# Kernel optimization log

Measured on AMD Instinct MI355X. Metric: run time of the kernel, lower is better.

Reference implementation:

```python
import jax, jax.numpy as jnp
import numpy as np

GAMMA = 0.5
LENS = 0.5
WINDOW = 10  # window_size from init

@jax.custom_vjp
def act_fun(x):
    # Heaviside forward, Gaussian surrogate backward (matches torch ActFun)
    return (x > 0).astype(x.dtype)

def _act_fwd(x):
    return act_fun(x), x

def _act_bwd(x, g):
    temp = jnp.exp(-x * x / (2 * LENS * LENS)) / (np.sqrt(2 * np.pi) * LENS)
    return (GAMMA * g * temp,)

act_fun.defvjp(_act_fwd, _act_bwd)

def mem_update(inputs, mem, thr):
    # decay_neu == 1
    mem = mem + inputs
    spike = act_fun(mem - thr)
    mem = mem * (1 - spike)
    neg = (mem < -thr).astype(mem.dtype)
    mem = mem * (1 - neg) - thr * neg
    return mem, spike

def setup_inputs() -> dict:
    key = jax.random.key(0)
    ks = jax.random.split(key, 6)
    B, T, D, H, O = 128, 100, 2048, 1024, 20
    return {
        "input": jax.random.normal(ks[0], (B, T, D), jnp.float32),
        "labels": jax.random.randint(ks[1], (B,), 0, O),
        "hidden_mem": jnp.zeros((B, H), jnp.float32),
        "hidden_spike": jnp.zeros((B, H), jnp.float32),
        "output_mem": jnp.zeros((B, O), jnp.float32),
        "output_spike": jnp.zeros((B, O), jnp.float32),
        "Wi2h": jax.random.normal(ks[2], (H, D), jnp.float32) / np.sqrt(D).astype(np.float32),
        "bi2h": jnp.zeros((H,), jnp.float32),
        "Wh2h": jax.random.normal(ks[3], (H, H), jnp.float32) / np.sqrt(H).astype(np.float32),
        "bh2h": jnp.zeros((H,), jnp.float32),
        "Wh2o": jax.random.normal(ks[4], (O, H), jnp.float32) / np.sqrt(H).astype(np.float32),
        "bh2o": jnp.zeros((O,), jnp.float32),
        "thr_h": jnp.ones((H,), jnp.float32),
        "thr_o": jnp.ones((O,), jnp.float32),
    }

def reference(input, labels, hidden_mem, hidden_spike, output_mem, output_spike,
              Wi2h, bi2h, Wh2h, bh2h, Wh2o, bh2o, thr_h, thr_o):
    B = input.shape[0]

    def step(carry, x_t):
        hm, hs, om, osp, osum = carry
        h_in = x_t @ Wi2h.T + bi2h + hs @ Wh2h.T + bh2h
        hm, hs = mem_update(h_in, hm, thr_h)
        om, osp = mem_update(hs @ Wh2o.T + bh2o, om, thr_o)
        osum = osum + osp
        nbr = (jnp.sum(osp) + jnp.sum(hs)) / B
        return (hm, hs, om, osp, osum), (hs, nbr)

    osum0 = jnp.zeros_like(output_spike)
    carry0 = (hidden_mem, hidden_spike, output_mem, output_spike, osum0)
    (hm, hs, om, osp, osum), (hs_t, nbr_events) = jax.lax.scan(
        step, carry0, jnp.swapaxes(input, 0, 1))  # scan over T

    hidden_spike_t = jnp.transpose(hs_t, (1, 2, 0))  # [B, H, T]
    # moving average over time windows (unfold + mean), stride 1
    c = jnp.cumsum(jnp.pad(hidden_spike_t, ((0, 0), (0, 0), (1, 0))), axis=2)
    hidden_spike_filt = (c[:, :, WINDOW:] - c[:, :, :-WINDOW]) / WINDOW  # [B,H,T-W+1]

    logp = jax.nn.log_softmax(osum, axis=1)
    predictions = jnp.argmax(logp, axis=1)[None, :]  # [1, B]
    loss = -jnp.mean(logp[jnp.arange(B), labels])  # NLLLoss on log_softmax
    return predictions, loss, nbr_events, hidden_spike_filt
```

## Files before the change

### kernel.cpp

```cpp
#include <hip/hip_runtime.h>
#include <hip/hip_bf16.h>
#include <cstdint>
#include <cstddef>

#define B_ 128
#define T_ 100
#define D_ 2048
#define H_ 1024
#define O_ 20
#define H2 512

__device__ inline void f4acc(float4& a, const float4 v) {
    a.x += v.x; a.y += v.y; a.z += v.z; a.w += v.w;
}

__global__ __launch_bounds__(256) void prep_kernel(const float* __restrict__ Wh2o,
                                                   float* __restrict__ W2oT,
                                                   float* __restrict__ nbr,
                                                   int* __restrict__ g_flag)
{
    int i = blockIdx.x * 256 + threadIdx.x;
    if (i < H_ * O_) {
        int hh = i / O_;
        int oo = i - hh * O_;
        W2oT[i] = Wh2o[oo * H_ + hh];
    }
    if (i < T_) nbr[i] = 0.0f;
    if (i < B_ * 2) g_flag[i] = 0;
}

__global__ __launch_bounds__(256) void transpose_kernel(const float* __restrict__ A,
                                                        float* __restrict__ AT)
{
    __shared__ float tile[32][33];
    int bx = blockIdx.x * 32, by = blockIdx.y * 32;
    int tx = threadIdx.x, ty = threadIdx.y;
#pragma unroll
    for (int i = 0; i < 32; i += 8)
        tile[ty + i][tx] = A[(size_t)(by + ty + i) * H_ + bx + tx];
    __syncthreads();
#pragma unroll
    for (int i = 0; i < 32; i += 8)
        AT[(size_t)(bx + ty + i) * H_ + by + tx] = tile[tx][ty + i];
}

__global__ __launch_bounds__(256) void gemm_xi_kernel(
    const float* __restrict__ X,
    const float* __restrict__ W,
    const float* __restrict__ bi2h,
    const float* __restrict__ bh2h,
    float* __restrict__ Xi)
{
    constexpr int BM = 128, BN = 128, BK = 16;
    __shared__ float As[BK][BM + 4];
    __shared__ float Bs[BK][BN + 4];
    const int tid = threadIdx.x;
    const int m0 = blockIdx.x * BM;
    const int n0 = blockIdx.y * BN;
    const int wave = tid >> 6;
    const int lane = tid & 63;
    const int tm = ((wave >> 1) << 3) | (lane >> 3);
    const int tn = ((wave & 1) << 3) | (lane & 7);
    const int ldr = tid >> 2;
    const int ldc = (tid & 3) << 2;

    float acc[8][8];
#pragma unroll
    for (int i = 0; i < 8; ++i)
#pragma unroll
        for (int j = 0; j < 8; ++j) acc[i][j] = 0.0f;

    for (int k0 = 0; k0 < D_; k0 += BK) {
#pragma unroll
        for (int p = 0; p < 2; ++p) {
            int r = ldr + p * 64;
            float4 v = *(const float4*)(X + (size_t)(m0 + r) * D_ + k0 + ldc);
            As[ldc + 0][r] = v.x; As[ldc + 1][r] = v.y;
            As[ldc + 2][r] = v.z; As[ldc + 3][r] = v.w;
        }
#pragma unroll
        for (int p = 0; p < 2; ++p) {
            int r = ldr + p * 64;
            float4 v = *(const float4*)(W + (size_t)(n0 + r) * D_ + k0 + ldc);
            Bs[ldc + 0][r] = v.x; Bs[ldc + 1][r] = v.y;
            Bs[ldc + 2][r] = v.z; Bs[ldc + 3][r] = v.w;
        }
        __syncthreads();
#pragma unroll
        for (int k = 0; k < BK; ++k) {
            float4 A0 = *(const float4*)&As[k][tm * 8];
            float4 A1 = *(const float4*)&As[k][tm * 8 + 4];
            float4 B0 = *(const float4*)&Bs[k][tn * 8];
            float4 B1 = *(const float4*)&Bs[k][tn * 8 + 4];
            float a[8] = {A0.x, A0.y, A0.z, A0.w, A1.x, A1.y, A1.z, A1.w};
            float bb[8] = {B0.x, B0.y, B0.z, B0.w, B1.x, B1.y, B1.z, B1.w};
#pragma unroll
            for (int i = 0; i < 8; ++i)
#pragma unroll
                for (int j = 0; j < 8; ++j) acc[i][j] += a[i] * bb[j];
        }
        __syncthreads();
    }

    float bsum[8];
#pragma unroll
    for (int j = 0; j < 8; ++j) {
        int n = n0 + tn * 8 + j;
        bsum[j] = bi2h[n] + bh2h[n];
    }
#pragma unroll
    for (int i = 0; i < 8; ++i) {
        size_t row = (size_t)(m0 + tm * 8 + i);
        float4 o0 = {acc[i][0] + bsum[0], acc[i][1] + bsum[1],
                     acc[i][2] + bsum[2], acc[i][3] + bsum[3]};
        float4 o1 = {acc[i][4] + bsum[4], acc[i][5] + bsum[5],
                     acc[i][6] + bsum[6], acc[i][7] + bsum[7]};
        *(float4*)(Xi + row * H_ + n0 + tn * 8)     = o0;
        *(float4*)(Xi + row * H_ + n0 + tn * 8 + 4) = o1;
    }
}

__global__ __launch_bounds__(512) void phase2_kernel(
    const float* __restrict__ Xi,
    const float* __restrict__ WT,
    const float* __restrict__ W2oT,
    const float* __restrict__ bh2o,
    const float* __restrict__ thr_h_g,
    const float* __restrict__ thr_o_g,
    const float* __restrict__ hm0,
    const float* __restrict__ hs0,
    const float* __restrict__ om0,
    unsigned long long* __restrict__ g_mask,
    int* __restrict__ g_flag,
    ulonglong2* __restrict__ spk,
    float* __restrict__ osum_out,
    float* __restrict__ nbr_acc)
{
    const int pair = blockIdx.x >> 1;
    const int half = blockIdx.x & 1;
    const int b = pair;
    const int tid = threadIdx.x;
    const int lane = tid & 63;
    const int wv = tid >> 6;
    const int h0 = half * H2;
    const int ph0 = h0 ^ H2;
    const int h = h0 + tid;

    __shared__ int   s_list[1024];
    __shared__ float4 s_red[4][128];
    __shared__ unsigned long long s_mask[16];
    __shared__ float s_opart[8][O_];
    __shared__ float s_om[O_], s_osum[O_], s_tho[O_], s_bo[O_];

    float hm = hm0[(size_t)b * H_ + h];
    const float thr = thr_h_g[h];

    if (half == 0 && tid < O_) {
        s_om[tid]   = om0[b * O_ + tid];
        s_osum[tid] = 0.0f;
        s_tho[tid]  = thr_o_g[tid];
        s_bo[tid]   = bh2o[tid];
    }

    {
        bool own = hs0[(size_t)b * H_ + h] > 0.5f;
        bool par = hs0[(size_t)b * H_ + ph0 + tid] > 0.5f;
        unsigned long long mo = __ballot(own), mp = __ballot(par);
        if (lane == 0) { s_mask[half * 8 + wv] = mo; s_mask[(half ^ 1) * 8 + wv] = mp; }
    }
    __syncthreads();

    int cnt_own;
    {
        const int ow = half * 8;
        int pc[8];
#pragma unroll
        for (int k = 0; k < 8; ++k) pc[k] = __popcll(s_mask[ow + k]);
        int basew = 0, tot = 0;
#pragma unroll
        for (int k = 0; k < 8; ++k) { if (k < wv) basew += pc[k]; tot += pc[k]; }
        cnt_own = tot;
        unsigned long long mw = s_mask[ow + wv];
        if ((mw >> lane) & 1ull)
            s_list[basew + __popcll(mw & ((1ull << lane) - 1ull))] = h;
    }
    __syncthreads();

    const float4* __restrict__ wt4b = (const float4*)WT + (h0 >> 2);
    const int g = tid >> 7;
    const int cid = tid & 127;
    const int fl_partner = pair * 2 + (half ^ 1);
    const int fl_self    = pair * 2 + half;
    unsigned long long bits0 = 0, bits1 = 0;

    for (int t = 0; t <= T_; ++t) {
        const bool full = (t < T_);
        float xi = 0.0f;
        if (full) xi = Xi[((size_t)b * T_ + t) * H_ + h];

        float4 c0 = {0,0,0,0}, c1 = {0,0,0,0}, c2 = {0,0,0,0}, c3 = {0,0,0,0};
        float4 c4 = {0,0,0,0}, c5 = {0,0,0,0}, c6 = {0,0,0,0}, c7 = {0,0,0,0};

        if (full) {
            const int c = cnt_own;
            int l = g;
            for (; l + 28 < c; l += 32) {
                int j0 = s_list[l],      j1 = s_list[l + 4];
                int j2 = s_list[l + 8],  j3 = s_list[l + 12];
                int j4 = s_list[l + 16], j5 = s_list[l + 20];
                int j6 = s_list[l + 24], j7 = s_list[l + 28];
                f4acc(c0, wt4b[(size_t)j0 * 256 + cid]);
                f4acc(c1, wt4b[(size_t)j1 * 256 + cid]);
                f4acc(c2, wt4b[(size_t)j2 * 256 + cid]);
                f4acc(c3, wt4b[(size_t)j3 * 256 + cid]);
                f4acc(c4, wt4b[(size_t)j4 * 256 + cid]);
                f4acc(c5, wt4b[(size_t)j5 * 256 + cid]);
                f4acc(c6, wt4b[(size_t)j6 * 256 + cid]);
                f4acc(c7, wt4b[(size_t)j7 * 256 + cid]);
            }
            for (; l < c; l += 4) f4acc(c0, wt4b[(size_t)s_list[l] * 256 + cid]);
        }

        if (t > 0 && tid == 0) {
            while (__hip_atomic_load(&g_flag[fl_partner], __ATOMIC_ACQUIRE,
                                     __HIP_MEMORY_SCOPE_AGENT) < t)
                __builtin_amdgcn_s_sleep(1);
        }
        __syncthreads();
        if (t > 0 && tid < 8) {
            const unsigned long long* pm =
                g_mask + (((size_t)(pair * 2 + ((t - 1) & 1)) * 2 + (half ^ 1)) * 8);
            s_mask[(half ^ 1) * 8 + tid] =
                __hip_atomic_load(&pm[tid], __ATOMIC_RELAXED, __HIP_MEMORY_SCOPE_AGENT);
        }
        __syncthreads();

        int cnt_p;
        {
            const int pw = (half ^ 1) * 8;
            int pc[8];
#pragma unroll
            for (int k = 0; k < 8; ++k) pc[k] = __popcll(s_mask[pw + k]);
            int basew = 0, tot = 0;
#pragma unroll
            for (int k = 0; k < 8; ++k) { if (k < wv) basew += pc[k]; tot += pc[k]; }
            cnt_p = tot;
            unsigned long long mw = s_mask[pw + wv];
            if ((mw >> lane) & 1ull)
                s_list[512 + basew + __popcll(mw & ((1ull << lane) - 1ull))] =
                    ph0 + wv * 64 + lane;
        }
        __syncthreads();

        if (full) {
            const int c = cnt_p;
            int l = g;
            for (; l + 28 < c; l += 32) {
                int j0 = s_list[512 + l],      j1 = s_list[512 + l + 4];
                int j2 = s_list[512 + l + 8],  j3 = s_list[512 + l + 12];
                int j4 = s_list[512 + l + 16], j5 = s_list[512 + l + 20];
                int j6 = s_list[512 + l + 24], j7 = s_list[512 + l + 28];
                f4acc(c0, wt4b[(size_t)j0 * 256 + cid]);
                f4acc(c1, wt4b[(size_t)j1 * 256 + cid]);
                f4acc(c2, wt4b[(size_t)j2 * 256 + cid]);
                f4acc(c3, wt4b[(size_t)j3 * 256 + cid]);
                f4acc(c4, wt4b[(size_t)j4 * 256 + cid]);
                f4acc(c5, wt4b[(size_t)j5 * 256 + cid]);
                f4acc(c6, wt4b[(size_t)j6 * 256 + cid]);
                f4acc(c7, wt4b[(size_t)j7 * 256 + cid]);
            }
            for (; l < c; l += 4) f4acc(c0, wt4b[(size_t)s_list[512 + l] * 256 + cid]);
        }

        if (half == 0 && t > 0 && lane < O_) {
            float op = 0.0f;
            for (int q = wv; q < cnt_own; q += 8) op += W2oT[s_list[q] * O_ + lane];
            for (int q = wv; q < cnt_p; q += 8)  op += W2oT[s_list[512 + q] * O_ + lane];
            s_opart[wv][lane] = op;
        }

        {
            f4acc(c0, c1); f4acc(c2, c3); f4acc(c4, c5); f4acc(c6, c7);
            f4acc(c0, c2); f4acc(c4, c6); f4acc(c0, c4);
            s_red[g][cid] = c0;
        }
        const int hidprev = cnt_own + cnt_p;
        __syncthreads();

        if (full) {
            const float* rf = (const float*)s_red;
            float val = rf[tid] + rf[512 + tid] + rf[1024 + tid] + rf[1536 + tid];
            hm += xi + val;
            bool sp = (hm - thr) > 0.0f;
            if (sp) hm = 0.0f;
            if (hm < -thr) hm = -thr;
            if (sp) { if (t < 64) bits0 |= 1ull << t; else bits1 |= 1ull << (t - 64); }
            unsigned long long m = __ballot(sp);
            if (lane == 0) {
                s_mask[half * 8 + wv] = m;
                unsigned long long* gm =
                    g_mask + (((size_t)(pair * 2 + (t & 1)) * 2 + half) * 8);
                __hip_atomic_store(&gm[wv], m, __ATOMIC_RELAXED,
                                   __HIP_MEMORY_SCOPE_AGENT);
            }
        }

        if (half == 0 && t > 0) {
            float osp_l = 0.0f;
            if (tid < O_) {
                float oin = s_bo[tid];
#pragma unroll
                for (int w = 0; w < 8; ++w) oin += s_opart[w][tid];
                float om = s_om[tid] + oin;
                float osp = ((om - s_tho[tid]) > 0.0f) ? 1.0f : 0.0f;
                if (osp > 0.5f) om = 0.0f;
                if (om < -s_tho[tid]) om = -s_tho[tid];
                s_om[tid] = om;
                s_osum[tid] += osp;
                osp_l = osp;
            }
            if (wv == 0) {
                float cc = osp_l;
                cc += __shfl_xor(cc, 1);  cc += __shfl_xor(cc, 2);
                cc += __shfl_xor(cc, 4);  cc += __shfl_xor(cc, 8);
                cc += __shfl_xor(cc, 16); cc += __shfl_xor(cc, 32);
                if (lane == 0)
                    atomicAdd(&nbr_acc[t - 1], cc + (float)hidprev);
            }
        }
        __syncthreads();
        if (full && tid == 0)
            __hip_atomic_store(&g_flag[fl_self], t + 1, __ATOMIC_RELEASE,
                               __HIP_MEMORY_SCOPE_AGENT);
        if (full) {
            const int ow = half * 8;
            int pc[8];
#pragma unroll
            for (int k = 0; k < 8; ++k) pc[k] = __popcll(s_mask[ow + k]);
            int basew = 0, tot = 0;
#pragma unroll
            for (int k = 0; k < 8; ++k) { if (k < wv) basew += pc[k]; tot += pc[k]; }
            cnt_own = tot;
            unsigned long long mw = s_mask[ow + wv];
            if ((mw >> lane) & 1ull)
                s_list[basew + __popcll(mw & ((1ull << lane) - 1ull))] = h;
        }
        __syncthreads();
    }

    ulonglong2 vv; vv.x = bits0; vv.y = bits1;
    spk[(size_t)b * H_ + h] = vv;
    if (half == 0 && tid < O_) osum_out[b * O_ + tid] = s_osum[tid];
}

__global__ __launch_bounds__(256) void filt_kernel(const ulonglong2* __restrict__ spk,
                                                   float* __restrict__ outf)
{
    int i = blockIdx.x * 256 + threadIdx.x;
    ulonglong2 v = spk[i];
    float* o = outf + (size_t)i * 91;
    int s = __popcll(v.x & 0x3FFull);
    o[0] = (float)s * 0.1f;
#pragma unroll 1
    for (int tau = 1; tau <= 90; ++tau) {
        int ta = tau + 9, tsb = tau - 1;
        int add = (ta < 64) ? (int)((v.x >> ta) & 1ull) : (int)((v.y >> (ta - 64)) & 1ull);
        int sub = (tsb < 64) ? (int)((v.x >> tsb) & 1ull) : (int)((v.y >> (tsb - 64)) & 1ull);
        s += add - sub;
        o[tau] = (float)s * 0.1f;
    }
}

__global__ __launch_bounds__(256) void final_kernel(const float* __restrict__ osum,
                                                    const int* __restrict__ labels,
                                                    float* __restrict__ dout)
{
    __shared__ float s_loss[B_];
    int tid = threadIdx.x;
    if (tid < B_) {
        int b = tid;
        float v[O_];
#pragma unroll
        for (int o = 0; o < O_; ++o) v[o] = osum[b * O_ + o];
        float mv = v[0];
        int am = 0;
#pragma unroll
        for (int o = 1; o < O_; ++o)
            if (v[o] > mv) { mv = v[o]; am = o; }
        float se = 0.0f;
#pragma unroll
        for (int o = 0; o < O_; ++o) se += expf(v[o] - mv);
        float lse = mv + logf(se);
        dout[b] = (float)am;
        s_loss[b] = v[labels[b]] - lse;
    }
    if (tid >= 128 && tid < 128 + T_) {
        dout[129 + (tid - 128)] *= (1.0f / (float)B_);
    }
    __syncthreads();
    if (tid == 0) {
        float s = 0.0f;
        for (int b = 0; b < B_; ++b) s += s_loss[b];
        dout[128] = -s / (float)B_;
    }
}

extern "C" void kernel_launch(void* const* d_in, const int* in_sizes, int n_in,
                              void* d_out, int out_size, void* d_ws, size_t ws_size,
                              hipStream_t stream)
{
    const float* input  = (const float*)d_in[0];
    const int*   labels = (const int*)d_in[1];
    const float* hm0    = (const float*)d_in[2];
    const float* hs0    = (const float*)d_in[3];
    const float* om0    = (const float*)d_in[4];
    const float* Wi2h   = (const float*)d_in[6];
    const float* bi2h   = (const float*)d_in[7];
    const float* Wh2h   = (const float*)d_in[8];
    const float* bh2h   = (const float*)d_in[9];
    const float* Wh2o   = (const float*)d_in[10];
    const float* bh2o   = (const float*)d_in[11];
    const float* thr_h  = (const float*)d_in[12];
    const float* thr_o  = (const float*)d_in[13];

    float* out  = (float*)d_out;
    float* nbr  = out + 129;
    float* filt = out + 229;

    char* ws = (char*)d_ws;
    float*      Xi     = (float*)(ws);
    float*      WT     = (float*)(ws + 52428800);
    float*      W2oT   = (float*)(ws + 56623104);
    ulonglong2* spk    = (ulonglong2*)(ws + 56705024);
    float*      osum   = (float*)(ws + 58802176);
    unsigned long long* g_mask = (unsigned long long*)(ws + 58812416);
    int*        g_flag  = (int*)(ws + 58845184);

    prep_kernel<<<80, 256, 0, stream>>>(Wh2o, W2oT, nbr, g_flag);
    transpose_kernel<<<dim3(32, 32), dim3(32, 8), 0, stream>>>(Wh2h, WT);
    gemm_xi_kernel<<<dim3(100, 8), 256, 0, stream>>>(input, Wi2h, bi2h, bh2h, Xi);
    phase2_kernel<<<256, 512, 0, stream>>>(Xi, WT, W2oT, bh2o, thr_h, thr_o,
                                           hm0, hs0, om0, g_mask, g_flag,
                                           spk, osum, nbr);
    filt_kernel<<<512, 256, 0, stream>>>(spk, filt);
    final_kernel<<<1, 256, 0, stream>>>(osum, labels, out);
}
```

Before: 2.027 ms.

## Fuse input GEMM into recurrent kernel with per-timestep readiness flags

Merges the input-projection GEMM and the recurrent scan into one persistent launch. The first 256 blocks run the recurrence and the other 800 each compute one timestep tile of Xi. Each GEMM block bumps a per-timestep counter, and the recurrent blocks spin on the counter for t+1 before moving on. This lets the recurrence start before the whole GEMM finishes, overlapping the two phases. The risks are forward-progress deadlock if recurrent blocks hold resources while GEMM blocks cannot schedule, plus a smaller and less efficient GEMM tile (128x128 with 512 threads per block) and contention on the compute units.

```diff
diff --git a/kernel.cpp b/kernel.cpp
--- a/kernel.cpp
+++ b/kernel.cpp
@@ -10,6 +10,12 @@
 #define O_ 20
 #define H2 512
 
+#define P2NB 256
+#define GEMM_NB 800
+#define XI_READY 8
+
+typedef float vfloat4 __attribute__((ext_vector_type(4)));
+
 __device__ inline void f4acc(float4& a, const float4 v) {
     a.x += v.x; a.y += v.y; a.z += v.z; a.w += v.w;
 }
@@ -17,7 +23,8 @@
 __global__ __launch_bounds__(256) void prep_kernel(const float* __restrict__ Wh2o,
                                                    float* __restrict__ W2oT,
                                                    float* __restrict__ nbr,
-                                                   int* __restrict__ g_flag)
+                                                   int* __restrict__ g_flag,
+                                                   int* __restrict__ xi_done)
 {
     int i = blockIdx.x * 256 + threadIdx.x;
     if (i < H_ * O_) {
@@ -25,7 +32,7 @@
         int oo = i - hh * O_;
         W2oT[i] = Wh2o[oo * H_ + hh];
     }
-    if (i < T_) nbr[i] = 0.0f;
+    if (i < T_) { nbr[i] = 0.0f; xi_done[i] = 0; }
     if (i < B_ * 2) g_flag[i] = 0;
 }
 
@@ -44,84 +51,79 @@
         AT[(size_t)(bx + ty + i) * H_ + by + tx] = tile[tx][ty + i];
 }
 
-__global__ __launch_bounds__(256) void gemm_xi_kernel(
+__device__ __forceinline__ void gemm_role(int g,
+    const float* __restrict__ X, const float* __restrict__ W,
+    const float* __restrict__ bi2h, const float* __restrict__ bh2h,
+    float* __restrict__ Xi, int* __restrict__ xi_done)
+{
+    __shared__ float As[16][132];
+    __shared__ float Bs[16][132];
+    const int t   = g >> 3;
+    const int n0  = (g & 7) << 7;
+    const int tid = threadIdx.x;
+    const int tm8 = (tid >> 5) << 3;
+    const int tn4 = (tid & 31) << 2;
+    const int ldr = tid >> 2;
+    const int ldc = (tid & 3) << 2;
+
+    const float* Xp = X + (size_t)ldr * (T_ * D_) + (size_t)t * D_ + ldc;
+    const float* Wp = W + (size_t)(n0 + ldr) * D_ + ldc;
+
+    float acc[8][4];
+#pragma unroll
+    for (int i = 0; i < 8; ++i)
+#pragma unroll
+        for (int j = 0; j < 4; ++j) acc[i][j] = 0.0f;
+
+    for (int k0 = 0; k0 < D_; k0 += 16) {
+        vfloat4 va = __builtin_nontemporal_load((const vfloat4*)(Xp + k0));
+        float4 vb = *(const float4*)(Wp + k0);
+        __syncthreads();
+        As[ldc + 0][ldr] = va.x; As[ldc + 1][ldr] = va.y;
+        As[ldc + 2][ldr] = va.z; As[ldc + 3][ldr] = va.w;
+        Bs[ldc + 0][ldr] = vb.x; Bs[ldc + 1][ldr] = vb.y;
+        Bs[ldc + 2][ldr] = vb.z; Bs[ldc + 3][ldr] = vb.w;
+        __syncthreads();
+#pragma unroll
+        for (int k = 0; k < 16; ++k) {
+            float4 A0 = *(const float4*)&As[k][tm8];
+            float4 A1 = *(const float4*)&As[k][tm8 + 4];
+            float4 B0 = *(const float4*)&Bs[k][tn4];
+            float a[8] = {A0.x, A0.y, A0.z, A0.w, A1.x, A1.y, A1.z, A1.w};
+            float b4[4] = {B0.x, B0.y, B0.z, B0.w};
+#pragma unroll
+            for (int i = 0; i < 8; ++i)
+#pragma unroll
+                for (int j = 0; j < 4; ++j) acc[i][j] += a[i] * b4[j];
+        }
+    }
+
+    float bs[4];
+#pragma unroll
+    for (int j = 0; j < 4; ++j) {
+        int n = n0 + tn4 + j;
+        bs[j] = bi2h[n] + bh2h[n];
+    }
+#pragma unroll
+    for (int i = 0; i < 8; ++i) {
+        size_t row = (size_t)(tm8 + i) * T_ + t;
+        vfloat4 o = {acc[i][0] + bs[0], acc[i][1] + bs[1],
+                     acc[i][2] + bs[2], acc[i][3] + bs[3]};
+        __builtin_nontemporal_store(o, (vfloat4*)(Xi + row * H_ + n0 + tn4));
+    }
+    __syncthreads();
+    if (tid == 0)
+        __hip_atomic_fetch_add(&xi_done[t], 1, __ATOMIC_RELEASE,
+                               __HIP_MEMORY_SCOPE_AGENT);
+}
+
+__global__ __launch_bounds__(512, 4) void mega_kernel(
     const float* __restrict__ X,
-    const float* __restrict__ W,
+    const float* __restrict__ Wi2h,
     const float* __restrict__ bi2h,
     const float* __restrict__ bh2h,
-    float* __restrict__ Xi)
-{
-    constexpr int BM = 128, BN = 128, BK = 16;
-    __shared__ float As[BK][BM + 4];
-    __shared__ float Bs[BK][BN + 4];
-    const int tid = threadIdx.x;
-    const int m0 = blockIdx.x * BM;
-    const int n0 = blockIdx.y * BN;
-    const int wave = tid >> 6;
-    const int lane = tid & 63;
-    const int tm = ((wave >> 1) << 3) | (lane >> 3);
-    const int tn = ((wave & 1) << 3) | (lane & 7);
-    const int ldr = tid >> 2;
-    const int ldc = (tid & 3) << 2;
-
-    float acc[8][8];
-#pragma unroll
-    for (int i = 0; i < 8; ++i)
-#pragma unroll
-        for (int j = 0; j < 8; ++j) acc[i][j] = 0.0f;
-
-    for (int k0 = 0; k0 < D_; k0 += BK) {
-#pragma unroll
-        for (int p = 0; p < 2; ++p) {
-            int r = ldr + p * 64;
-            float4 v = *(const float4*)(X + (size_t)(m0 + r) * D_ + k0 + ldc);
-            As[ldc + 0][r] = v.x; As[ldc + 1][r] = v.y;
-            As[ldc + 2][r] = v.z; As[ldc + 3][r] = v.w;
-        }
-#pragma unroll
-        for (int p = 0; p < 2; ++p) {
-            int r = ldr + p * 64;
-            float4 v = *(const float4*)(W + (size_t)(n0 + r) * D_ + k0 + ldc);
-            Bs[ldc + 0][r] = v.x; Bs[ldc + 1][r] = v.y;
-            Bs[ldc + 2][r] = v.z; Bs[ldc + 3][r] = v.w;
-        }
-        __syncthreads();
-#pragma unroll
-        for (int k = 0; k < BK; ++k) {
-            float4 A0 = *(const float4*)&As[k][tm * 8];
-            float4 A1 = *(const float4*)&As[k][tm * 8 + 4];
-            float4 B0 = *(const float4*)&Bs[k][tn * 8];
-            float4 B1 = *(const float4*)&Bs[k][tn * 8 + 4];
-            float a[8] = {A0.x, A0.y, A0.z, A0.w, A1.x, A1.y, A1.z, A1.w};
-            float bb[8] = {B0.x, B0.y, B0.z, B0.w, B1.x, B1.y, B1.z, B1.w};
-#pragma unroll
-            for (int i = 0; i < 8; ++i)
-#pragma unroll
-                for (int j = 0; j < 8; ++j) acc[i][j] += a[i] * bb[j];
-        }
-        __syncthreads();
-    }
-
-    float bsum[8];
-#pragma unroll
-    for (int j = 0; j < 8; ++j) {
-        int n = n0 + tn * 8 + j;
-        bsum[j] = bi2h[n] + bh2h[n];
-    }
-#pragma unroll
-    for (int i = 0; i < 8; ++i) {
-        size_t row = (size_t)(m0 + tm * 8 + i);
-        float4 o0 = {acc[i][0] + bsum[0], acc[i][1] + bsum[1],
-                     acc[i][2] + bsum[2], acc[i][3] + bsum[3]};
-        float4 o1 = {acc[i][4] + bsum[4], acc[i][5] + bsum[5],
-                     acc[i][6] + bsum[6], acc[i][7] + bsum[7]};
-        *(float4*)(Xi + row * H_ + n0 + tn * 8)     = o0;
-        *(float4*)(Xi + row * H_ + n0 + tn * 8 + 4) = o1;
-    }
-}
-
-__global__ __launch_bounds__(512) void phase2_kernel(
-    const float* __restrict__ Xi,
+    float* __restrict__ Xi,
+    int* __restrict__ xi_done,
     const float* __restrict__ WT,
     const float* __restrict__ W2oT,
     const float* __restrict__ bh2o,
@@ -136,6 +138,11 @@
     float* __restrict__ osum_out,
     float* __restrict__ nbr_acc)
 {
+    if (blockIdx.x >= P2NB) {
+        gemm_role(blockIdx.x - P2NB, X, Wi2h, bi2h, bh2h, Xi, xi_done);
+        return;
+    }
+
     const int pair = blockIdx.x >> 1;
     const int half = blockIdx.x & 1;
     const int b = pair;
@@ -183,6 +190,11 @@
         unsigned long long mw = s_mask[ow + wv];
         if ((mw >> lane) & 1ull)
             s_list[basew + __popcll(mw & ((1ull << lane) - 1ull))] = h;
+    }
+    if (tid == 0) {
+        while (__hip_atomic_load(&xi_done[0], __ATOMIC_ACQUIRE,
+                                 __HIP_MEMORY_SCOPE_AGENT) < XI_READY)
+            __builtin_amdgcn_s_sleep(1);
     }
     __syncthreads();
 
@@ -221,10 +233,17 @@
             for (; l < c; l += 4) f4acc(c0, wt4b[(size_t)s_list[l] * 256 + cid]);
         }
 
-        if (t > 0 && tid == 0) {
-            while (__hip_atomic_load(&g_flag[fl_partner], __ATOMIC_ACQUIRE,
-                                     __HIP_MEMORY_SCOPE_AGENT) < t)
-                __builtin_amdgcn_s_sleep(1);
+        if (tid == 0) {
+            if (t > 0) {
+                while (__hip_atomic_load(&g_flag[fl_partner], __ATOMIC_ACQUIRE,
+                                         __HIP_MEMORY_SCOPE_AGENT) < t)
+                    __builtin_amdgcn_s_sleep(1);
+            }
+            if (t + 1 < T_) {
+                while (__hip_atomic_load(&xi_done[t + 1], __ATOMIC_ACQUIRE,
+                                         __HIP_MEMORY_SCOPE_AGENT) < XI_READY)
+                    __builtin_amdgcn_s_sleep(1);
+            }
         }
         __syncthreads();
         if (t > 0 && tid < 8) {
@@ -435,13 +454,14 @@
     float*      osum   = (float*)(ws + 58802176);
     unsigned long long* g_mask = (unsigned long long*)(ws + 58812416);
     int*        g_flag  = (int*)(ws + 58845184);
-
-    prep_kernel<<<80, 256, 0, stream>>>(Wh2o, W2oT, nbr, g_flag);
+    int*        xi_done = (int*)(ws + 58846208);
+
+    prep_kernel<<<80, 256, 0, stream>>>(Wh2o, W2oT, nbr, g_flag, xi_done);
     transpose_kernel<<<dim3(32, 32), dim3(32, 8), 0, stream>>>(Wh2h, WT);
-    gemm_xi_kernel<<<dim3(100, 8), 256, 0, stream>>>(input, Wi2h, bi2h, bh2h, Xi);
-    phase2_kernel<<<256, 512, 0, stream>>>(Xi, WT, W2oT, bh2o, thr_h, thr_o,
-                                           hm0, hs0, om0, g_mask, g_flag,
-                                           spk, osum, nbr);
+    mega_kernel<<<P2NB + GEMM_NB, 512, 0, stream>>>(
+        input, Wi2h, bi2h, bh2h, Xi, xi_done,
+        WT, W2oT, bh2o, thr_h, thr_o, hm0, hs0, om0,
+        g_mask, g_flag, spk, osum, nbr);
     filt_kernel<<<512, 256, 0, stream>>>(spk, filt);
     final_kernel<<<1, 256, 0, stream>>>(osum, labels, out);
 }
```

Result: slower. 2.793 ms (+37.8%).
